# Optimization experiments

Measured on AMD Instinct MI355X. Metric: run time of the kernel, lower is better.

The kernel has to match this reference:

```python
import jax, jax.numpy as jnp
import numpy as np

B, T, D, H, E, DLAT = 4, 2048, 512, 8, 32, 64
DH = D // H  # head_dim = 64


def rmsnorm(x, gamma, eps=1e-6):
    norm = jnp.sqrt(jnp.mean(jnp.square(x), axis=-1, keepdims=True) + eps)
    return gamma * (x / norm)


def apply_rope(x):
    # x: (B, T, H, Dh); rotate-half style RoPE over last dim
    _, t, _, d = x.shape
    inv_freq = 1.0 / (10000.0 ** (jnp.arange(0, d, 2, dtype=jnp.float32) / d))
    freqs = jnp.outer(jnp.arange(t, dtype=jnp.float32), inv_freq)  # (T, d/2)
    sin = jnp.sin(freqs)[None, :, None, :]
    cos = jnp.cos(freqs)[None, :, None, :]
    x1, x2 = jnp.split(x, 2, axis=-1)
    return jnp.concatenate([x1 * cos - x2 * sin, x1 * sin + x2 * cos], axis=-1)


def setup_inputs() -> dict:
    key = jax.random.key(0)
    ks = jax.random.split(key, 8)
    s = lambda fan_in: 1.0 / np.sqrt(fan_in)
    return {
        "x": jax.random.normal(ks[0], (B, T, D), jnp.float32),
        "gamma1": jnp.ones((D,), jnp.float32),
        "gamma2": jnp.ones((D,), jnp.float32),
        "wq": jax.random.normal(ks[1], (D, D), jnp.float32) * s(D),
        "bq": jnp.zeros((D,), jnp.float32),
        "wkd": jax.random.normal(ks[2], (D, DLAT), jnp.float32) * s(D),
        "bkd": jnp.zeros((DLAT,), jnp.float32),
        "wku": jax.random.normal(ks[3], (DLAT, 2 * D), jnp.float32) * s(DLAT),
        "bku": jnp.zeros((2 * D,), jnp.float32),
        "wo": jax.random.normal(ks[4], (D, D), jnp.float32) * s(D),
        "bo": jnp.zeros((D,), jnp.float32),
        "wg": jax.random.normal(ks[5], (D, E), jnp.float32) * s(D),
        "bg": jnp.zeros((E,), jnp.float32),
        "expert_w": jax.random.normal(ks[6], (E, D, D), jnp.float32) * s(D),
    }


def reference(x, gamma1, gamma2, wq, bq, wkd, bkd, wku, bku, wo, bo, wg, bg, expert_w):
    b, t, d = x.shape
    # --- MLA attention branch ---
    h = rmsnorm(x, gamma1)
    q = (h @ wq + bq).reshape(b, t, H, DH)
    kv = ((h @ wkd + bkd) @ wku + bku).reshape(b, t, H, 2 * DH)
    k, v = jnp.split(kv, 2, axis=-1)
    q = apply_rope(q)
    k = apply_rope(k)
    # NOTE (faithful to source): attention is across HEADS per timestep -> (B,T,H,H)
    att = jnp.einsum("bthd,btgd->bthg", q, k) / jnp.sqrt(jnp.float32(DH))
    att = jax.nn.softmax(att, axis=-1)
    out = jnp.einsum("bthg,btgd->bthd", att, v).reshape(b, t, d)
    x = x + (out @ wo + bo)
    # --- dense soft-MoE branch ---
    h2 = rmsnorm(x, gamma2)
    gate = jax.nn.softmax(h2 @ wg + bg, axis=-1)  # (B, T, E)
    moe = jnp.einsum("btd,edf,bte->btf", h2, expert_w, gate)
    return x + moe
```

## Files before the change

kernel.cpp:

```cpp
#include <hip/hip_runtime.h>
#include <hip/hip_bf16.h>

#define B_ 4
#define T_ 2048
#define D_ 512
#define H_ 8
#define E_ 32
#define DLAT_ 64
#define DH_ 64
#define M_ (B_*T_)

typedef unsigned short u16;
typedef unsigned int u32;
typedef __bf16 bf16x8 __attribute__((ext_vector_type(8)));
typedef float f32x4 __attribute__((ext_vector_type(4)));

__device__ __forceinline__ float bf2f(u16 u) {
    union { u32 i; float f; } c; c.i = ((u32)u) << 16; return c.f;
}
__device__ __forceinline__ u16 f2bf(float f) {
    union { float f; u32 i; } c; c.f = f;
    u32 x = c.i; x += 0x7fffu + ((x >> 16) & 1u);
    return (u16)(x >> 16);
}
__device__ __forceinline__ u32 pack2(float a, float b) {
    return (u32)f2bf(a) | ((u32)f2bf(b) << 16);
}

__global__ __launch_bounds__(256) void transpose_f2b(
    const float* __restrict__ src, u16* __restrict__ dst,
    int R, int C, int dstStride, long srcBatchStride, int dstBatchOff)
{
    __shared__ float tile[32][33];
    const int z = blockIdx.z;
    const float* s = src + (long)z * srcBatchStride;
    const int c0 = blockIdx.x * 32, r0 = blockIdx.y * 32;
    const int tx = threadIdx.x, ty = threadIdx.y;
#pragma unroll
    for (int i = 0; i < 32; i += 8) {
        int r = r0 + ty + i, c = c0 + tx;
        if (r < R && c < C) tile[ty + i][tx] = s[(long)r * C + c];
    }
    __syncthreads();
#pragma unroll
    for (int i = 0; i < 32; i += 8) {
        int c = c0 + ty + i, r = r0 + tx;
        if (r < R && c < C)
            dst[(long)c * dstStride + (long)z * dstBatchOff + r] = f2bf(tile[tx][ty + i]);
    }
}

__global__ __launch_bounds__(256) void rmsnorm_k(
    const float* __restrict__ x, const float* __restrict__ gamma,
    float* __restrict__ of, u16* __restrict__ ob)
{
    const size_t row = blockIdx.x;
    const int t = threadIdx.x;
    const float* xr = x + row * D_;
    float2 v = *(const float2*)(xr + 2 * t);
    float ss = v.x * v.x + v.y * v.y;
#pragma unroll
    for (int off = 1; off < 64; off <<= 1) ss += __shfl_xor(ss, off, 64);
    __shared__ float wsum[4];
    if ((t & 63) == 0) wsum[t >> 6] = ss;
    __syncthreads();
    float tot = wsum[0] + wsum[1] + wsum[2] + wsum[3];
    float inv = rsqrtf(tot * (1.0f / D_) + 1e-6f);
    float o0 = v.x * inv * gamma[2 * t];
    float o1 = v.y * inv * gamma[2 * t + 1];
    if (of) *(float2*)(of + row * D_ + 2 * t) = make_float2(o0, o1);
    if (ob) *(u32*)(ob + row * D_ + 2 * t) = pack2(o0, o1);
}

template<bool GATED>
__global__ __launch_bounds__(512, 4) void gemm8w(
    const u16* __restrict__ A, const u16* __restrict__ Bt,
    const float* __restrict__ gate, const float* __restrict__ bias,
    const float* __restrict__ resid, float* __restrict__ outF,
    u16* __restrict__ outB, int Ndim, int strideA,
    int kPerSplit, long splitOutOff)
{
    __shared__ __align__(16) u16 lA[128][72];
    __shared__ __align__(16) u16 lB[128][72];
    const int t = threadIdx.x;
    const int lane = t & 63, wid = t >> 6;
    const int wr = wid >> 2, wc = wid & 3;
    const int rowBase = blockIdx.x * 128;
    const int colBase = blockIdx.y * 128;
    const int z = blockIdx.z;
    const int kStart = z * kPerSplit;
    const int kEnd = kStart + kPerSplit;
    if (outF) outF += (size_t)z * splitOutOff;
    const int K = GATED ? (E_ * 512) : kPerSplit * (int)gridDim.z;
    const int srow = t >> 3;
    const int scol = (t & 7) * 8;
    const int l15 = lane & 15;
    const int kreg = (lane >> 4) * 8;

    f32x4 acc[4][2] = {};

    for (int kb = kStart; kb < kEnd; kb += 64) {
        const int akb = GATED ? (kb & 511) : kb;
#pragma unroll
        for (int i = 0; i < 2; ++i) {
            int r = srow + 64 * i;
            if constexpr (GATED) {
                const int e = kb >> 9;
                float g = gate[(size_t)(rowBase + r) * E_ + e];
                int4 raw = *(const int4*)(A + (size_t)(rowBase + r) * strideA + akb + scol);
                u32 wv[4] = {(u32)raw.x, (u32)raw.y, (u32)raw.z, (u32)raw.w};
                int4 o;
                o.x = (int)pack2(bf2f((u16)(wv[0] & 0xffff)) * g, bf2f((u16)(wv[0] >> 16)) * g);
                o.y = (int)pack2(bf2f((u16)(wv[1] & 0xffff)) * g, bf2f((u16)(wv[1] >> 16)) * g);
                o.z = (int)pack2(bf2f((u16)(wv[2] & 0xffff)) * g, bf2f((u16)(wv[2] >> 16)) * g);
                o.w = (int)pack2(bf2f((u16)(wv[3] & 0xffff)) * g, bf2f((u16)(wv[3] >> 16)) * g);
                *(int4*)(&lA[r][scol]) = o;
            } else {
                *(int4*)(&lA[r][scol]) =
                    *(const int4*)(A + (size_t)(rowBase + r) * strideA + akb + scol);
            }
            *(int4*)(&lB[r][scol]) =
                *(const int4*)(Bt + (size_t)(colBase + r) * K + kb + scol);
        }
        __syncthreads();
#pragma unroll
        for (int kk = 0; kk < 64; kk += 32) {
            const int ko = kk + kreg;
            bf16x8 af[4], bfr[2];
#pragma unroll
            for (int mi = 0; mi < 4; ++mi)
                af[mi] = *(const bf16x8*)(&lA[wr * 64 + mi * 16 + l15][ko]);
#pragma unroll
            for (int ni = 0; ni < 2; ++ni)
                bfr[ni] = *(const bf16x8*)(&lB[wc * 32 + ni * 16 + l15][ko]);
#pragma unroll
            for (int mi = 0; mi < 4; ++mi)
#pragma unroll
                for (int ni = 0; ni < 2; ++ni)
                    acc[mi][ni] = __builtin_amdgcn_mfma_f32_16x16x32_bf16(
                        af[mi], bfr[ni], acc[mi][ni], 0, 0, 0);
        }
        __syncthreads();
    }
#pragma unroll
    for (int mi = 0; mi < 4; ++mi)
#pragma unroll
        for (int ni = 0; ni < 2; ++ni)
#pragma unroll
            for (int r = 0; r < 4; ++r) {
                int grow = rowBase + wr * 64 + mi * 16 + (lane >> 4) * 4 + r;
                int gcol = colBase + wc * 32 + ni * 16 + l15;
                float v = acc[mi][ni][r];
                if (bias)  v += bias[gcol];
                if (resid) v += resid[(size_t)grow * Ndim + gcol];
                if (outF)  outF[(size_t)grow * Ndim + gcol] = v;
                if (outB)  outB[(size_t)grow * Ndim + gcol] = f2bf(v);
            }
}

__global__ __launch_bounds__(256) void gemm_bt(
    const u16* __restrict__ A, const u16* __restrict__ Bt,
    const float* __restrict__ bias, float* __restrict__ outF,
    u16* __restrict__ outB, int Ndim, int K)
{
    __shared__ __align__(16) u16 lA[128][72];
    __shared__ __align__(16) u16 lB[64][72];
    const int t = threadIdx.x;
    const int lane = t & 63, wid = t >> 6;
    const int rowBase = blockIdx.x * 128;
    const int colBase = blockIdx.y * 64;
    const int srow = t >> 3;
    const int skb = (t & 7) * 8;
    const int l15 = lane & 15;
    const int kreg = (lane >> 4) * 8;

    f32x4 accT[2][4] = {};

    for (int kb = 0; kb < K; kb += 64) {
#pragma unroll
        for (int i = 0; i < 4; ++i) {
            int r = srow + 32 * i;
            size_t grow = (size_t)(rowBase + r);
            *(int4*)(&lA[r][skb]) = *(const int4*)(A + grow * (size_t)K + kb + skb);
        }
#pragma unroll
        for (int i = 0; i < 2; ++i) {
            int n = srow + 32 * i;
            int gn = colBase + n;
            int4 v = {0, 0, 0, 0};
            if (gn < Ndim) v = *(const int4*)(Bt + (size_t)gn * K + kb + skb);
            *(int4*)(&lB[n][skb]) = v;
        }
        __syncthreads();
#pragma unroll
        for (int kk = 0; kk < 64; kk += 32) {
            const int ko = kk + kreg;
            bf16x8 af[2], bfr[4];
            af[0] = *(const bf16x8*)(&lA[wid * 32 + l15][ko]);
            af[1] = *(const bf16x8*)(&lA[wid * 32 + 16 + l15][ko]);
#pragma unroll
            for (int ni = 0; ni < 4; ++ni)
                bfr[ni] = *(const bf16x8*)(&lB[ni * 16 + l15][ko]);
#pragma unroll
            for (int mi = 0; mi < 2; ++mi)
#pragma unroll
                for (int ni = 0; ni < 4; ++ni)
                    accT[mi][ni] = __builtin_amdgcn_mfma_f32_16x16x32_bf16(
                        af[mi], bfr[ni], accT[mi][ni], 0, 0, 0);
        }
        __syncthreads();
    }
#pragma unroll
    for (int mi = 0; mi < 2; ++mi)
#pragma unroll
        for (int ni = 0; ni < 4; ++ni)
#pragma unroll
            for (int r = 0; r < 4; ++r) {
                int grow = rowBase + wid * 32 + mi * 16 + (lane >> 4) * 4 + r;
                int gcol = colBase + ni * 16 + l15;
                if (gcol < Ndim) {
                    float v = accT[mi][ni][r];
                    if (bias)  v += bias[gcol];
                    if (outF)  outF[(size_t)grow * Ndim + gcol] = v;
                    if (outB)  outB[(size_t)grow * Ndim + gcol] = f2bf(v);
                }
            }
}

__global__ __launch_bounds__(256) void reduce3_k(
    const float* __restrict__ a, const float* __restrict__ b,
    const float* __restrict__ c, float* __restrict__ o, int n4)
{
    int i = blockIdx.x * 256 + threadIdx.x;
    const int stride = gridDim.x * 256;
    for (; i < n4; i += stride) {
        float4 va = ((const float4*)a)[i];
        float4 vb = ((const float4*)b)[i];
        float4 vc = ((const float4*)c)[i];
        float4 r;
        r.x = va.x + vb.x + vc.x;
        r.y = va.y + vb.y + vc.y;
        r.z = va.z + vb.z + vc.z;
        r.w = va.w + vb.w + vc.w;
        ((float4*)o)[i] = r;
    }
}

__global__ __launch_bounds__(64) void attn_k(
    const float* __restrict__ q, const float* __restrict__ kv,
    u16* __restrict__ out)
{
    const int tok = blockIdx.x;
    const int tpos = tok & (T_ - 1);
    const int l = threadIdx.x;
    __shared__ float sq[8][65], sk[8][65], sv[8][65];
    __shared__ float satt[8][9];
    const int h = l >> 3;
    const int j0 = (l & 7) * 4;
    const float* qr = q + (size_t)tok * 512;
    const float* kr = kv + (size_t)tok * 1024;
#pragma unroll
    for (int jj = 0; jj < 4; ++jj) {
        int j = j0 + jj;
        float inv = exp2f(-(float)j * (13.287712379549449f / 32.0f));
        float ang = (float)tpos * inv;
        float sn, cs;
        sincosf(ang, &sn, &cs);
        float q1 = qr[h * 64 + j], q2 = qr[h * 64 + 32 + j];
        sq[h][j] = q1 * cs - q2 * sn;
        sq[h][j + 32] = q1 * sn + q2 * cs;
        float k1 = kr[h * 128 + j], k2 = kr[h * 128 + 32 + j];
        sk[h][j] = k1 * cs - k2 * sn;
        sk[h][j + 32] = k1 * sn + k2 * cs;
        sv[h][j] = kr[h * 128 + 64 + j];
        sv[h][j + 32] = kr[h * 128 + 96 + j];
    }
    __syncthreads();
    const int g = l & 7;
    float s = 0.f;
#pragma unroll 8
    for (int c = 0; c < 64; ++c) s += sq[h][c] * sk[g][c];
    s *= 0.125f;
    float m = s;
#pragma unroll
    for (int off = 4; off; off >>= 1) m = fmaxf(m, __shfl_xor(m, off, 8));
    float p = __expf(s - m);
    float den = p;
#pragma unroll
    for (int off = 4; off; off >>= 1) den += __shfl_xor(den, off, 8);
    satt[h][g] = p / den;
    __syncthreads();
    const int c8 = (l & 7) * 8;
    float o[8] = {};
#pragma unroll
    for (int gg = 0; gg < 8; ++gg) {
        float a = satt[h][gg];
#pragma unroll
        for (int i = 0; i < 8; ++i) o[i] += a * sv[gg][c8 + i];
    }
    int4 pk;
    pk.x = pack2(o[0], o[1]); pk.y = pack2(o[2], o[3]);
    pk.z = pack2(o[4], o[5]); pk.w = pack2(o[6], o[7]);
    *(int4*)(out + (size_t)tok * 512 + h * 64 + c8) = pk;
}

__global__ __launch_bounds__(256) void gate_k(
    const u16* __restrict__ h2, const float* __restrict__ wg,
    const float* __restrict__ bg, float* __restrict__ gate)
{
    __shared__ float sh[8][516];
    const int t = threadIdx.x;
    const size_t tok0 = (size_t)blockIdx.x * 8;
#pragma unroll
    for (int i = 0; i < 2; ++i) {
        int chunk = t + i * 256;
        int row = chunk >> 6;
        int c8 = (chunk & 63) * 8;
        int4 raw = *(const int4*)(h2 + (tok0 + row) * 512 + c8);
        u32 wv[4] = {(u32)raw.x, (u32)raw.y, (u32)raw.z, (u32)raw.w};
#pragma unroll
        for (int j = 0; j < 4; ++j) {
            sh[row][c8 + 2 * j] = bf2f((u16)(wv[j] & 0xffff));
            sh[row][c8 + 2 * j + 1] = bf2f((u16)(wv[j] >> 16));
        }
    }
    __syncthreads();
    const int e = t & 31;
    const int tl = t >> 5;
    float acc = bg[e];
#pragma unroll 4
    for (int d = 0; d < 512; ++d) acc += sh[tl][d] * wg[d * 32 + e];
    float m = acc;
#pragma unroll
    for (int off = 16; off; off >>= 1) m = fmaxf(m, __shfl_xor(m, off, 32));
    float p = __expf(acc - m);
    float ssum = p;
#pragma unroll
    for (int off = 16; off; off >>= 1) ssum += __shfl_xor(ssum, off, 32);
    gate[(tok0 + tl) * 32 + e] = p / ssum;
}

extern "C" void kernel_launch(void* const* d_in, const int* in_sizes, int n_in,
                              void* d_out, int out_size, void* d_ws, size_t ws_size,
                              hipStream_t stream)
{
    const float* x      = (const float*)d_in[0];
    const float* gamma1 = (const float*)d_in[1];
    const float* gamma2 = (const float*)d_in[2];
    const float* wq     = (const float*)d_in[3];
    const float* bq     = (const float*)d_in[4];
    const float* wkd    = (const float*)d_in[5];
    const float* bkd    = (const float*)d_in[6];
    const float* wku    = (const float*)d_in[7];
    const float* bku    = (const float*)d_in[8];
    const float* wo     = (const float*)d_in[9];
    const float* bo     = (const float*)d_in[10];
    const float* wg     = (const float*)d_in[11];
    const float* bg     = (const float*)d_in[12];
    const float* expw   = (const float*)d_in[13];

    char* w = (char*)d_ws;
    size_t off = 0;
    auto alloc = [&](size_t bytes) -> void* {
        void* p = w + off; off += (bytes + 255) & ~(size_t)255; return p;
    };
    u16*   h_b    = (u16*)alloc((size_t)M_ * D_ * 2);
    u16*   kd_b   = (u16*)alloc((size_t)M_ * DLAT_ * 2);
    u16*   at_b   = (u16*)alloc((size_t)M_ * D_ * 2);
    u16*   h2_b   = (u16*)alloc((size_t)M_ * D_ * 2);
    float* q_f    = (float*)alloc((size_t)M_ * D_ * 4);
    float* kv_f   = (float*)alloc((size_t)M_ * 2 * D_ * 4);
    float* x1_f   = (float*)alloc((size_t)M_ * D_ * 4);
    float* gate_f = (float*)alloc((size_t)M_ * E_ * 4);
    u16*   wqT    = (u16*)alloc((size_t)D_ * D_ * 2);
    u16*   wkdT   = (u16*)alloc((size_t)D_ * DLAT_ * 2);
    u16*   wkuT   = (u16*)alloc((size_t)DLAT_ * 2 * D_ * 2);
    u16*   woT    = (u16*)alloc((size_t)D_ * D_ * 2);
    u16*   expT   = (u16*)alloc((size_t)E_ * D_ * D_ * 2);
    (void)ws_size; (void)in_sizes; (void)n_in; (void)out_size;

    float* part0 = kv_f;
    float* part1 = kv_f + (size_t)M_ * D_;

    dim3 tb(32, 8);
    transpose_f2b<<<dim3(16, 16, 1), tb, 0, stream>>>(wq,  wqT,  512, 512, 512, 0L, 0);
    transpose_f2b<<<dim3(2, 16, 1),  tb, 0, stream>>>(wkd, wkdT, 512, 64,  512, 0L, 0);
    transpose_f2b<<<dim3(32, 2, 1),  tb, 0, stream>>>(wku, wkuT, 64, 1024, 64,  0L, 0);
    transpose_f2b<<<dim3(16, 16, 1), tb, 0, stream>>>(wo,  woT,  512, 512, 512, 0L, 0);
    transpose_f2b<<<dim3(16, 16, 32), tb, 0, stream>>>(expw, expT, 512, 512, 16384,
                                                       (long)512 * 512, 512);
    rmsnorm_k<<<M_, 256, 0, stream>>>(x, gamma1, nullptr, h_b);
    gemm8w<false><<<dim3(64, 4, 1), 512, 0, stream>>>(h_b, wqT, nullptr, bq,
                                                      nullptr, q_f, nullptr, 512, 512, 512, 0L);
    gemm_bt<<<dim3(64, 1), 256, 0, stream>>>(h_b, wkdT, bkd, nullptr, kd_b, 64, 512);
    gemm8w<false><<<dim3(64, 8, 1), 512, 0, stream>>>(kd_b, wkuT, nullptr, bku,
                                                      nullptr, kv_f, nullptr, 1024, 64, 64, 0L);
    attn_k<<<M_, 64, 0, stream>>>(q_f, kv_f, at_b);
    gemm8w<false><<<dim3(64, 4, 1), 512, 0, stream>>>(at_b, woT, nullptr, bo,
                                                      x, x1_f, nullptr, 512, 512, 512, 0L);
    rmsnorm_k<<<M_, 256, 0, stream>>>(x1_f, gamma2, nullptr, h2_b);
    gate_k<<<M_ / 8, 256, 0, stream>>>(h2_b, wg, bg, gate_f);
    gemm8w<true><<<dim3(64, 4, 2), 512, 0, stream>>>(h2_b, expT, gate_f, nullptr,
                                                     nullptr, part0, nullptr, 512, 512,
                                                     8192, (long)M_ * D_);
    reduce3_k<<<2048, 256, 0, stream>>>(x1_f, part0, part1, (float*)d_out,
                                        M_ * D_ / 4);
}
```

Before: 402.3 us.

## Retile MoE GEMM to 256x128 blocks with 4-way split-K and precompute RoPE table

The gated MoE GEMM moves into a dedicated kernel with 256x128 output tiles, a 4x4 MFMA accumulator per wave and 4-way split-K. This raises arithmetic intensity per staged tile and halves B-tile reloads per output row. The partials go into the contiguous q_f/kv_f/pext workspace, and a 5-input reduction adds them to the residual. Separately, RoPE sin/cos values are precomputed once into a table instead of calling sincosf per token in the attention kernel. The costs are more partial-sum traffic in the reduction and higher LDS use per block, which may limit occupancy.

New measurement: 367.6 us. -8.6%, faster.

```diff
diff --git a/kernel.cpp b/kernel.cpp
--- a/kernel.cpp
+++ b/kernel.cpp
@@ -72,13 +72,10 @@
     if (ob) *(u32*)(ob + row * D_ + 2 * t) = pack2(o0, o1);
 }
 
-template<bool GATED>
 __global__ __launch_bounds__(512, 4) void gemm8w(
     const u16* __restrict__ A, const u16* __restrict__ Bt,
-    const float* __restrict__ gate, const float* __restrict__ bias,
-    const float* __restrict__ resid, float* __restrict__ outF,
-    u16* __restrict__ outB, int Ndim, int strideA,
-    int kPerSplit, long splitOutOff)
+    const float* __restrict__ bias, const float* __restrict__ resid,
+    float* __restrict__ outF, u16* __restrict__ outB, int Ndim, int strideA, int K)
 {
     __shared__ __align__(16) u16 lA[128][72];
     __shared__ __align__(16) u16 lB[128][72];
@@ -87,11 +84,6 @@
     const int wr = wid >> 2, wc = wid & 3;
     const int rowBase = blockIdx.x * 128;
     const int colBase = blockIdx.y * 128;
-    const int z = blockIdx.z;
-    const int kStart = z * kPerSplit;
-    const int kEnd = kStart + kPerSplit;
-    if (outF) outF += (size_t)z * splitOutOff;
-    const int K = GATED ? (E_ * 512) : kPerSplit * (int)gridDim.z;
     const int srow = t >> 3;
     const int scol = (t & 7) * 8;
     const int l15 = lane & 15;
@@ -99,26 +91,12 @@
 
     f32x4 acc[4][2] = {};
 
-    for (int kb = kStart; kb < kEnd; kb += 64) {
-        const int akb = GATED ? (kb & 511) : kb;
+    for (int kb = 0; kb < K; kb += 64) {
 #pragma unroll
         for (int i = 0; i < 2; ++i) {
             int r = srow + 64 * i;
-            if constexpr (GATED) {
-                const int e = kb >> 9;
-                float g = gate[(size_t)(rowBase + r) * E_ + e];
-                int4 raw = *(const int4*)(A + (size_t)(rowBase + r) * strideA + akb + scol);
-                u32 wv[4] = {(u32)raw.x, (u32)raw.y, (u32)raw.z, (u32)raw.w};
-                int4 o;
-                o.x = (int)pack2(bf2f((u16)(wv[0] & 0xffff)) * g, bf2f((u16)(wv[0] >> 16)) * g);
-                o.y = (int)pack2(bf2f((u16)(wv[1] & 0xffff)) * g, bf2f((u16)(wv[1] >> 16)) * g);
-                o.z = (int)pack2(bf2f((u16)(wv[2] & 0xffff)) * g, bf2f((u16)(wv[2] >> 16)) * g);
-                o.w = (int)pack2(bf2f((u16)(wv[3] & 0xffff)) * g, bf2f((u16)(wv[3] >> 16)) * g);
-                *(int4*)(&lA[r][scol]) = o;
-            } else {
-                *(int4*)(&lA[r][scol]) =
-                    *(const int4*)(A + (size_t)(rowBase + r) * strideA + akb + scol);
-            }
+            *(int4*)(&lA[r][scol]) =
+                *(const int4*)(A + (size_t)(rowBase + r) * strideA + kb + scol);
             *(int4*)(&lB[r][scol]) =
                 *(const int4*)(Bt + (size_t)(colBase + r) * K + kb + scol);
         }
@@ -155,6 +133,82 @@
                 if (resid) v += resid[(size_t)grow * Ndim + gcol];
                 if (outF)  outF[(size_t)grow * Ndim + gcol] = v;
                 if (outB)  outB[(size_t)grow * Ndim + gcol] = f2bf(v);
+            }
+}
+
+#define KPS_ 4096
+__global__ __launch_bounds__(512, 4) void moe256(
+    const u16* __restrict__ A, const u16* __restrict__ Bt,
+    const float* __restrict__ gate, float* __restrict__ part)
+{
+    __shared__ __align__(16) u16 lA[256][72];
+    __shared__ __align__(16) u16 lB[128][72];
+    const int t = threadIdx.x;
+    const int lane = t & 63, wid = t >> 6;
+    const int wr = wid >> 1, wc = wid & 1;
+    const int rowBase = blockIdx.x * 256;
+    const int colBase = blockIdx.y * 128;
+    const int z = blockIdx.z;
+    const int kStart = z * KPS_;
+    float* outF = part + (size_t)z * M_ * D_;
+    const int srow = t >> 3;
+    const int scol = (t & 7) * 8;
+    const int l15 = lane & 15;
+    const int kreg = (lane >> 4) * 8;
+
+    f32x4 acc[4][4] = {};
+
+    for (int kb = kStart; kb < kStart + KPS_; kb += 64) {
+        const int akb = kb & 511;
+        const int e = kb >> 9;
+#pragma unroll
+        for (int i = 0; i < 4; ++i) {
+            int r = srow + 64 * i;
+            float g = gate[(size_t)(rowBase + r) * E_ + e];
+            int4 raw = *(const int4*)(A + (size_t)(rowBase + r) * 512 + akb + scol);
+            u32 wv[4] = {(u32)raw.x, (u32)raw.y, (u32)raw.z, (u32)raw.w};
+            int4 o;
+            o.x = (int)pack2(bf2f((u16)(wv[0] & 0xffff)) * g, bf2f((u16)(wv[0] >> 16)) * g);
+            o.y = (int)pack2(bf2f((u16)(wv[1] & 0xffff)) * g, bf2f((u16)(wv[1] >> 16)) * g);
+            o.z = (int)pack2(bf2f((u16)(wv[2] & 0xffff)) * g, bf2f((u16)(wv[2] >> 16)) * g);
+            o.w = (int)pack2(bf2f((u16)(wv[3] & 0xffff)) * g, bf2f((u16)(wv[3] >> 16)) * g);
+            *(int4*)(&lA[r][scol]) = o;
+        }
+#pragma unroll
+        for (int i = 0; i < 2; ++i) {
+            int r = srow + 64 * i;
+            *(int4*)(&lB[r][scol]) =
+                *(const int4*)(Bt + (size_t)(colBase + r) * (E_ * 512) + kb + scol);
+        }
+        __syncthreads();
+#pragma unroll
+        for (int kk = 0; kk < 64; kk += 32) {
+            const int ko = kk + kreg;
+            bf16x8 af[4], bfr[4];
+#pragma unroll
+            for (int mi = 0; mi < 4; ++mi)
+                af[mi] = *(const bf16x8*)(&lA[wr * 64 + mi * 16 + l15][ko]);
+#pragma unroll
+            for (int ni = 0; ni < 4; ++ni)
+                bfr[ni] = *(const bf16x8*)(&lB[wc * 64 + ni * 16 + l15][ko]);
+#pragma unroll
+            for (int mi = 0; mi < 4; ++mi)
+#pragma unroll
+                for (int ni = 0; ni < 4; ++ni)
+                    acc[mi][ni] = __builtin_amdgcn_mfma_f32_16x16x32_bf16(
+                        af[mi], bfr[ni], acc[mi][ni], 0, 0, 0);
+        }
+        __syncthreads();
+    }
+#pragma unroll
+    for (int mi = 0; mi < 4; ++mi)
+#pragma unroll
+        for (int ni = 0; ni < 4; ++ni)
+#pragma unroll
+            for (int r = 0; r < 4; ++r) {
+                int grow = rowBase + wr * 64 + mi * 16 + (lane >> 4) * 4 + r;
+                int gcol = colBase + wc * 64 + ni * 16 + l15;
+                outF[(size_t)grow * D_ + gcol] = acc[mi][ni][r];
             }
 }
 
@@ -227,28 +281,42 @@
             }
 }
 
-__global__ __launch_bounds__(256) void reduce3_k(
-    const float* __restrict__ a, const float* __restrict__ b,
-    const float* __restrict__ c, float* __restrict__ o, int n4)
+__global__ __launch_bounds__(256) void reduce5_k(
+    const float* __restrict__ a, const float* __restrict__ p,
+    float* __restrict__ o, int n4)
 {
     int i = blockIdx.x * 256 + threadIdx.x;
     const int stride = gridDim.x * 256;
-    for (; i < n4; i += stride) {
+    const int n4b = n4;
+    for (; i < n4b; i += stride) {
         float4 va = ((const float4*)a)[i];
-        float4 vb = ((const float4*)b)[i];
-        float4 vc = ((const float4*)c)[i];
+        float4 v0 = ((const float4*)p)[i];
+        float4 v1 = ((const float4*)p)[i + n4b];
+        float4 v2 = ((const float4*)p)[i + 2 * n4b];
+        float4 v3 = ((const float4*)p)[i + 3 * n4b];
         float4 r;
-        r.x = va.x + vb.x + vc.x;
-        r.y = va.y + vb.y + vc.y;
-        r.z = va.z + vb.z + vc.z;
-        r.w = va.w + vb.w + vc.w;
+        r.x = va.x + v0.x + v1.x + v2.x + v3.x;
+        r.y = va.y + v0.y + v1.y + v2.y + v3.y;
+        r.z = va.z + v0.z + v1.z + v2.z + v3.z;
+        r.w = va.w + v0.w + v1.w + v2.w + v3.w;
         ((float4*)o)[i] = r;
     }
+}
+
+__global__ __launch_bounds__(256) void rope_build(float2* __restrict__ tab)
+{
+    int i = blockIdx.x * 256 + threadIdx.x;
+    int tpos = i >> 5, j = i & 31;
+    float inv = exp2f(-(float)j * (13.287712379549449f / 32.0f));
+    float ang = (float)tpos * inv;
+    float sn, cs;
+    sincosf(ang, &sn, &cs);
+    tab[i] = make_float2(cs, sn);
 }
 
 __global__ __launch_bounds__(64) void attn_k(
     const float* __restrict__ q, const float* __restrict__ kv,
-    u16* __restrict__ out)
+    const float2* __restrict__ rope, u16* __restrict__ out)
 {
     const int tok = blockIdx.x;
     const int tpos = tok & (T_ - 1);
@@ -262,10 +330,8 @@
 #pragma unroll
     for (int jj = 0; jj < 4; ++jj) {
         int j = j0 + jj;
-        float inv = exp2f(-(float)j * (13.287712379549449f / 32.0f));
-        float ang = (float)tpos * inv;
-        float sn, cs;
-        sincosf(ang, &sn, &cs);
+        float2 cssn = rope[tpos * 32 + j];
+        float cs = cssn.x, sn = cssn.y;
         float q1 = qr[h * 64 + j], q2 = qr[h * 64 + 32 + j];
         sq[h][j] = q1 * cs - q2 * sn;
         sq[h][j + 32] = q1 * sn + q2 * cs;
@@ -370,17 +436,18 @@
     u16*   h2_b   = (u16*)alloc((size_t)M_ * D_ * 2);
     float* q_f    = (float*)alloc((size_t)M_ * D_ * 4);
     float* kv_f   = (float*)alloc((size_t)M_ * 2 * D_ * 4);
+    float* pext   = (float*)alloc((size_t)M_ * D_ * 4);
     float* x1_f   = (float*)alloc((size_t)M_ * D_ * 4);
     float* gate_f = (float*)alloc((size_t)M_ * E_ * 4);
+    float2* rope_t = (float2*)alloc((size_t)T_ * 32 * 8);
     u16*   wqT    = (u16*)alloc((size_t)D_ * D_ * 2);
     u16*   wkdT   = (u16*)alloc((size_t)D_ * DLAT_ * 2);
     u16*   wkuT   = (u16*)alloc((size_t)DLAT_ * 2 * D_ * 2);
     u16*   woT    = (u16*)alloc((size_t)D_ * D_ * 2);
     u16*   expT   = (u16*)alloc((size_t)E_ * D_ * D_ * 2);
-    (void)ws_size; (void)in_sizes; (void)n_in; (void)out_size;
-
-    float* part0 = kv_f;
-    float* part1 = kv_f + (size_t)M_ * D_;
+    (void)ws_size; (void)in_sizes; (void)n_in; (void)out_size; (void)pext;
+
+    float* parts = q_f;
 
     dim3 tb(32, 8);
     transpose_f2b<<<dim3(16, 16, 1), tb, 0, stream>>>(wq,  wqT,  512, 512, 512, 0L, 0);
@@ -389,20 +456,18 @@
     transpose_f2b<<<dim3(16, 16, 1), tb, 0, stream>>>(wo,  woT,  512, 512, 512, 0L, 0);
     transpose_f2b<<<dim3(16, 16, 32), tb, 0, stream>>>(expw, expT, 512, 512, 16384,
                                                        (long)512 * 512, 512);
+    rope_build<<<(T_ * 32) / 256, 256, 0, stream>>>(rope_t);
     rmsnorm_k<<<M_, 256, 0, stream>>>(x, gamma1, nullptr, h_b);
-    gemm8w<false><<<dim3(64, 4, 1), 512, 0, stream>>>(h_b, wqT, nullptr, bq,
-                                                      nullptr, q_f, nullptr, 512, 512, 512, 0L);
+    gemm8w<<<dim3(64, 4), 512, 0, stream>>>(h_b, wqT, bq, nullptr, q_f, nullptr,
+                                            512, 512, 512);
     gemm_bt<<<dim3(64, 1), 256, 0, stream>>>(h_b, wkdT, bkd, nullptr, kd_b, 64, 512);
-    gemm8w<false><<<dim3(64, 8, 1), 512, 0, stream>>>(kd_b, wkuT, nullptr, bku,
-                                                      nullptr, kv_f, nullptr, 1024, 64, 64, 0L);
-    attn_k<<<M_, 64, 0, stream>>>(q_f, kv_f, at_b);
-    gemm8w<false><<<dim3(64, 4, 1), 512, 0, stream>>>(at_b, woT, nullptr, bo,
-                                                      x, x1_f, nullptr, 512, 512, 512, 0L);
+    gemm8w<<<dim3(64, 8), 512, 0, stream>>>(kd_b, wkuT, bku, nullptr, kv_f, nullptr,
+                                            1024, 64, 64);
+    attn_k<<<M_, 64, 0, stream>>>(q_f, kv_f, rope_t, at_b);
+    gemm8w<<<dim3(64, 4), 512, 0, stream>>>(at_b, woT, bo, x, x1_f, nullptr,
+                                            512, 512, 512);
     rmsnorm_k<<<M_, 256, 0, stream>>>(x1_f, gamma2, nullptr, h2_b);
     gate_k<<<M_ / 8, 256, 0, stream>>>(h2_b, wg, bg, gate_f);
-    gemm8w<true><<<dim3(64, 4, 2), 512, 0, stream>>>(h2_b, expT, gate_f, nullptr,
-                                                     nullptr, part0, nullptr, 512, 512,
-                                                     8192, (long)M_ * D_);
-    reduce3_k<<<2048, 256, 0, stream>>>(x1_f, part0, part1, (float*)d_out,
-                                        M_ * D_ / 4);
-}
+    moe256<<<dim3(32, 4, 4), 512, 0, stream>>>(h2_b, expT, gate_f, parts);
+    reduce5_k<<<2048, 256, 0, stream>>>(x1_f, parts, (float*)d_out, M_ * D_ / 4);
+}
```
